# Kernel tuning notes

Measured on AMD Instinct MI355X. Metric: run time of the kernel, lower is better.

Reference implementation:

```python
import jax, jax.numpy as jnp
import numpy as np

HIDDEN = 1024

def _init_linear(key, in_f, out_f):
    kw, kb = jax.random.split(key)
    bound = 1.0 / np.sqrt(in_f)
    W = jax.random.uniform(kw, (out_f, in_f), jnp.float32, -bound, bound)
    b = jax.random.uniform(kb, (out_f,), jnp.float32, -bound, bound)
    return W, b

def setup_inputs() -> dict:
    key = jax.random.key(0)
    ks = jax.random.split(key, 6)
    x = jax.random.normal(ks[0], (64, 512, 512), jnp.float32)
    # layer 0: input_size=512, hidden=1024
    W_rz0, b_rz0 = _init_linear(ks[1], 512 + HIDDEN, 2 * HIDDEN)
    W_n0, b_n0 = _init_linear(ks[2], 512 + HIDDEN, HIDDEN)
    # layer 1: input_size=hidden=1024
    W_rz1, b_rz1 = _init_linear(ks[3], HIDDEN + HIDDEN, 2 * HIDDEN)
    W_n1, b_n1 = _init_linear(ks[4], HIDDEN + HIDDEN, HIDDEN)
    # final fc: hidden -> output_size=512
    W_fc, b_fc = _init_linear(ks[5], HIDDEN, 512)
    return {"x": x, "W_rz0": W_rz0, "b_rz0": b_rz0, "W_n0": W_n0, "b_n0": b_n0,
            "W_rz1": W_rz1, "b_rz1": b_rz1, "W_n1": W_n1, "b_n1": b_n1,
            "W_fc": W_fc, "b_fc": b_fc}

def _gru_cell(xt, h, W_rz, b_rz, W_n, b_n):
    ih = jnp.concatenate([xt, h], axis=1)                 # [B, in+H]
    rz = ih @ W_rz.T + b_rz                               # [B, 2H]
    r, z = jnp.split(rz, 2, axis=1)
    r = jax.nn.sigmoid(r)
    z = jax.nn.sigmoid(z)
    ih_n = jnp.concatenate([xt, r * h], axis=1)
    n = jnp.tanh(ih_n @ W_n.T + b_n)
    return (1.0 - z) * n + z * h

def reference(x, W_rz0, b_rz0, W_n0, b_n0, W_rz1, b_rz1, W_n1, b_n1, W_fc, b_fc):
    B = x.shape[0]
    h0 = jnp.zeros((B, HIDDEN), x.dtype)
    h1 = jnp.zeros((B, HIDDEN), x.dtype)

    def step(carry, xt):
        h0, h1 = carry
        h0 = _gru_cell(xt, h0, W_rz0, b_rz0, W_n0, b_n0)
        h1 = _gru_cell(h0, h1, W_rz1, b_rz1, W_n1, b_n1)
        return (h0, h1), None

    xs = jnp.swapaxes(x, 0, 1)                            # [T, B, in]
    (h0, h1), _ = jax.lax.scan(step, (h0, h1), xs)
    # original returns outputs[:, -1, :] == fc(final hidden of last layer)
    return h1 @ W_fc.T + b_fc
```

## Files before the change

kernel.cpp:

```cpp
#include <hip/hip_runtime.h>
#include <math.h>

typedef _Float16 h8 __attribute__((ext_vector_type(8)));
typedef float f4 __attribute__((ext_vector_type(4)));

#define H 1024

#define OFF_WRZ0 0ull
#define OFF_WN0  6291456ull
#define OFF_WRZ1 9437184ull
#define OFF_WN1  17825792ull
#define OFF_H0BF 22020096ull
#define OFF_H1BF 22282240ull
#define OFF_RH0  22544384ull
#define OFF_RH1  22675456ull
#define OFF_H0F  22806528ull
#define OFF_H1F  23068672ull
#define OFF_Z0F  23330816ull
#define OFF_Z1F  23592960ull
#define OFF_CNT  23855104ull
#define OFF_INFO 23855168ull
#define OFF_CCNT 23855680ull
#define OFF_CP   23859200ull
#define CP_XCD_STRIDE 1048576ull
#define ZERO_WORDS 458960

__device__ __forceinline__ unsigned long long llc_ld64(const void* p) {
  return __hip_atomic_load((const unsigned long long*)p, __ATOMIC_RELAXED, __HIP_MEMORY_SCOPE_AGENT);
}
__device__ __forceinline__ void llc_st64(void* p, unsigned long long v) {
  __hip_atomic_store((unsigned long long*)p, v, __ATOMIC_RELAXED, __HIP_MEMORY_SCOPE_AGENT);
}
__device__ __forceinline__ void llc_st32(void* p, unsigned v) {
  __hip_atomic_store((unsigned*)p, v, __ATOMIC_RELAXED, __HIP_MEMORY_SCOPE_AGENT);
}
__device__ __forceinline__ unsigned long long pack2f(float a, float b) {
  union { float f[2]; unsigned long long u; } x; x.f[0] = a; x.f[1] = b; return x.u;
}
__device__ __forceinline__ void unpack2f(unsigned long long v, float& a, float& b) {
  union { unsigned long long u; float f[2]; } x; x.u = v; a = x.f[0]; b = x.f[1];
}
__device__ __forceinline__ unsigned packh2(float a, float b) {
  union { _Float16 h[2]; unsigned u; } x; x.h[0] = (_Float16)a; x.h[1] = (_Float16)b; return x.u;
}

__global__ __launch_bounds__(256) void prep_kernel(
    const float* __restrict__ wrz0f, const float* __restrict__ wn0f,
    const float* __restrict__ wrz1f, const float* __restrict__ wn1f,
    _Float16* __restrict__ wrz0, _Float16* __restrict__ wn0,
    _Float16* __restrict__ wrz1, _Float16* __restrict__ wn1,
    unsigned* __restrict__ zbase) {
  size_t i = (size_t)blockIdx.x * blockDim.x + threadIdx.x;
  size_t stride = (size_t)gridDim.x * blockDim.x;
  for (size_t k = i; k < 2048ull * 1536ull; k += stride) wrz0[k] = (_Float16)wrz0f[k];
  for (size_t k = i; k < 1024ull * 1536ull; k += stride) wn0[k]  = (_Float16)wn0f[k];
  for (size_t k = i; k < 2048ull * 2048ull; k += stride) wrz1[k] = (_Float16)wrz1f[k];
  for (size_t k = i; k < 1024ull * 2048ull; k += stride) wn1[k]  = (_Float16)wn1f[k];
  for (size_t k = i; k < (size_t)ZERO_WORDS; k += stride) zbase[k] = 0u;
}

__device__ __forceinline__ void wait_ge(unsigned long long* c, unsigned long long tgt) {
  if (threadIdx.x == 0) {
    while (__hip_atomic_load(c, __ATOMIC_RELAXED, __HIP_MEMORY_SCOPE_AGENT) < tgt)
      __builtin_amdgcn_s_sleep(2);
  }
  __syncthreads();
}
__device__ __forceinline__ void signal(unsigned long long* c) {
  __syncthreads();
  if (threadIdx.x == 0)
    __hip_atomic_fetch_add(c, 1ull, __ATOMIC_RELAXED, __HIP_MEMORY_SCOPE_AGENT);
}

__device__ __forceinline__ void copy_tensor(const void* __restrict__ master,
                                            void* __restrict__ cp,
                                            int rank, int m,
                                            unsigned long long* ccnt,
                                            unsigned long long target) {
  const unsigned long long* src = (const unsigned long long*)master;
  unsigned long long* dst = (unsigned long long*)cp;
  for (int u = rank * 1024 + (int)threadIdx.x; u < 16384; u += m * 1024)
    dst[u] = llc_ld64(src + u);
  __syncthreads();
  if (threadIdx.x == 0) {
    __hip_atomic_fetch_add(ccnt, 1ull, __ATOMIC_RELAXED, __HIP_MEMORY_SCOPE_AGENT);
    while (__hip_atomic_load(ccnt, __ATOMIC_RELAXED, __HIP_MEMORY_SCOPE_AGENT) < target)
      __builtin_amdgcn_s_sleep(2);
  }
  __syncthreads();
  asm volatile("buffer_inv sc0" ::: "memory");
}

template<int NT>
__device__ __forceinline__ void gemm_cp(const _Float16* __restrict__ A,
                                        const _Float16* const* wps, int coff, f4* acc) {
  const int lane = threadIdx.x & 63, wv = threadIdx.x >> 6;
  const int kwq = wv & 3, mw = wv >> 2;
  const int rsub = lane & 15, kg = (lane >> 4) << 3;
  const _Float16* ap = A + (size_t)(mw * 16 + rsub) * 1024 + kwq * 256 + kg;
#pragma unroll
  for (int k0 = 0; k0 < 256; k0 += 32) {
    h8 a = *(const h8*)(ap + k0);
    int kc = coff + kwq * 256 + k0 + kg;
#pragma unroll
    for (int c = 0; c < NT; ++c) {
      h8 wf = *(const h8*)(wps[c] + kc);
      acc[c] = __builtin_amdgcn_mfma_f32_16x16x32_f16(a, wf, acc[c], 0, 0, 0);
    }
  }
}

__device__ __forceinline__ void gemm_x(const float* __restrict__ x, int t,
                                       const _Float16* __restrict__ wr0,
                                       const _Float16* __restrict__ wr1,
                                       const _Float16* __restrict__ wn,
                                       f4* aRZ, f4* aN) {
  const int lane = threadIdx.x & 63, wv = threadIdx.x >> 6;
  const int kwq = wv & 3, mw = wv >> 2;
  const int rsub = lane & 15, kg = (lane >> 4) << 3;
  const float* xb = x + (size_t)(mw * 16 + rsub) * 262144 + (size_t)t * 512;
#pragma unroll
  for (int k0 = 0; k0 < 128; k0 += 32) {
    int k = kwq * 128 + k0 + kg;
    float4 f0 = *(const float4*)(xb + k);
    float4 f1 = *(const float4*)(xb + k + 4);
    h8 a;
    a[0] = (_Float16)f0.x; a[1] = (_Float16)f0.y; a[2] = (_Float16)f0.z; a[3] = (_Float16)f0.w;
    a[4] = (_Float16)f1.x; a[5] = (_Float16)f1.y; a[6] = (_Float16)f1.z; a[7] = (_Float16)f1.w;
    aRZ[0] = __builtin_amdgcn_mfma_f32_16x16x32_f16(a, *(const h8*)(wr0 + k), aRZ[0], 0, 0, 0);
    aRZ[1] = __builtin_amdgcn_mfma_f32_16x16x32_f16(a, *(const h8*)(wr1 + k), aRZ[1], 0, 0, 0);
    aN[0]  = __builtin_amdgcn_mfma_f32_16x16x32_f16(a, *(const h8*)(wn + k),  aN[0], 0, 0, 0);
  }
}

template<int NT>
__device__ __forceinline__ void red_write(float* __restrict__ red, const f4* acc) {
  const int lane = threadIdx.x & 63, wv = threadIdx.x >> 6;
  const int kwq = wv & 3, mw = wv >> 2;
  const int rsub = lane & 15, rg = lane >> 4;
#pragma unroll
  for (int c = 0; c < NT; ++c)
#pragma unroll
    for (int j = 0; j < 4; ++j)
      red[(size_t)(kwq * 64 + mw * 16 + rg * 4 + j) * 33 + c * 16 + rsub] = acc[c][j];
}

__device__ __forceinline__ void reduce_rz(const float* __restrict__ red, int cb,
    const float* __restrict__ bias, const float* __restrict__ hf,
    _Float16* __restrict__ rh, float* __restrict__ zf) {
  const int tid = threadIdx.x;
  const int row = tid >> 4, cp = (tid & 15) << 1;
  float v0 = 0.f, v1 = 0.f;
#pragma unroll
  for (int q = 0; q < 4; ++q) {
    const float* rr = red + (size_t)(q * 64 + row) * 33 + cp;
    v0 += rr[0]; v1 += rr[1];
  }
  v0 += bias[cb + cp]; v1 += bias[cb + cp + 1];
  float s0 = 1.f / (1.f + expf(-v0));
  float s1 = 1.f / (1.f + expf(-v1));
  if (cb < 1024) {
    float h0v, h1v;
    unpack2f(llc_ld64(hf + (size_t)row * H + cb + cp), h0v, h1v);
    llc_st32(rh + (size_t)row * H + cb + cp, packh2(s0 * h0v, s1 * h1v));
  } else {
    llc_st64(zf + (size_t)row * H + (cb - 1024) + cp, pack2f(s0, s1));
  }
}

__device__ __forceinline__ void reduce_n(const float* __restrict__ red, int nb,
    const float* __restrict__ bias, const float* __restrict__ zf,
    float* __restrict__ hf, _Float16* __restrict__ hb) {
  const int tid = threadIdx.x;
  if (tid < 512) {
    const int row = tid >> 3, cp = (tid & 7) << 1;
    float v0 = 0.f, v1 = 0.f;
#pragma unroll
    for (int q = 0; q < 4; ++q) {
      const float* rr = red + (size_t)(q * 64 + row) * 33 + cp;
      v0 += rr[0]; v1 += rr[1];
    }
    v0 += bias[nb + cp]; v1 += bias[nb + cp + 1];
    float n0 = tanhf(v0), n1 = tanhf(v1);
    float z0, z1, h0v, h1v;
    unpack2f(llc_ld64(zf + (size_t)row * H + nb + cp), z0, z1);
    unpack2f(llc_ld64(hf + (size_t)row * H + nb + cp), h0v, h1v);
    float o0 = (1.f - z0) * n0 + z0 * h0v;
    float o1 = (1.f - z1) * n1 + z1 * h1v;
    llc_st64(hf + (size_t)row * H + nb + cp, pack2f(o0, o1));
    llc_st32(hb + (size_t)row * H + nb + cp, packh2(o0, o1));
  }
}

__global__ __launch_bounds__(1024) void gru_main(const float* __restrict__ x,
    const _Float16* __restrict__ wrz0, const _Float16* __restrict__ wn0,
    const _Float16* __restrict__ wrz1, const _Float16* __restrict__ wn1,
    const float* __restrict__ brz0, const float* __restrict__ bn0,
    const float* __restrict__ brz1, const float* __restrict__ bn1,
    _Float16* __restrict__ h0bf, _Float16* __restrict__ h1bf,
    _Float16* __restrict__ rh0, _Float16* __restrict__ rh1,
    float* __restrict__ h0f, float* __restrict__ h1f,
    float* __restrict__ z0f, float* __restrict__ z1f,
    unsigned long long* __restrict__ cnt, unsigned* __restrict__ info,
    unsigned long long* __restrict__ ccnt_all, char* __restrict__ cpbase) {
  __shared__ float red[256 * 33];
  __shared__ int sh_meta[5];
  const int bid = blockIdx.x;
  const int tid = threadIdx.x;
  const int myrole = (bid < 64) ? 0 : 1;

  if (tid == 0) {
    unsigned xcc;
    asm volatile("s_getreg_b32 %0, hwreg(HW_REG_XCC_ID)" : "=s"(xcc));
    xcc &= 7u;
    llc_st32(&info[bid], 0x80000000u | xcc);
    asm volatile("s_waitcnt vmcnt(0)" ::: "memory");
    __hip_atomic_fetch_add(&cnt[4], 1ull, __ATOMIC_RELAXED, __HIP_MEMORY_SCOPE_AGENT);
    while (__hip_atomic_load(&cnt[4], __ATOMIC_RELAXED, __HIP_MEMORY_SCOPE_AGENT) < 128ull)
      __builtin_amdgcn_s_sleep(2);
    int rankA = 0, mA = 0, rankR = 0, mR = 0;
    for (int b = 0; b < 128; ++b) {
      unsigned v = (unsigned)__hip_atomic_load(&info[b], __ATOMIC_RELAXED, __HIP_MEMORY_SCOPE_AGENT);
      if ((v & 7u) == xcc) {
        int role = (b < 64) ? 0 : 1;
        if (b < bid) rankA++;
        mA++;
        if (role == myrole) { if (b < bid) rankR++; mR++; }
      }
    }
    sh_meta[0] = (int)xcc; sh_meta[1] = rankA; sh_meta[2] = mA;
    sh_meta[3] = rankR; sh_meta[4] = mR;
  }
  __syncthreads();
  const int xcd = sh_meta[0], rankA = sh_meta[1], mA = sh_meta[2];
  const int rankR = sh_meta[3], mR = sh_meta[4];
  unsigned long long* cc = ccnt_all + (size_t)xcd * 4;
  char* cpx = cpbase + (size_t)xcd * CP_XCD_STRIDE;
  _Float16* cpH0[2]  = {(_Float16*)(cpx + 0*131072), (_Float16*)(cpx + 1*131072)};
  _Float16* cpRH0[2] = {(_Float16*)(cpx + 2*131072), (_Float16*)(cpx + 3*131072)};
  _Float16* cpH1[2]  = {(_Float16*)(cpx + 4*131072), (_Float16*)(cpx + 5*131072)};
  _Float16* cpRH1[2] = {(_Float16*)(cpx + 6*131072), (_Float16*)(cpx + 7*131072)};
  const int rsub = tid & 15;

  if (myrole == 0) {
    const int cb = bid * 32, nb = bid * 16;
    const _Float16* wpsRZ[2] = { wrz0 + (size_t)(cb + rsub) * 1536,
                                 wrz0 + (size_t)(cb + 16 + rsub) * 1536 };
    const _Float16* wpsN[1] = { wn0 + (size_t)(nb + rsub) * 1536 };
    for (int t = 0; t < 512; ++t) {
      f4 aRZ[2] = { f4{0.f,0.f,0.f,0.f}, f4{0.f,0.f,0.f,0.f} };
      f4 aN[1] = { f4{0.f,0.f,0.f,0.f} };
      gemm_x(x, t, wpsRZ[0], wpsRZ[1], wpsN[0], aRZ, aN);
      wait_ge(&cnt[1], 64ull * (unsigned long long)t);
      if (t >= 1) {
        copy_tensor(h0bf + (size_t)((t - 1) & 1) * 65536, cpH0[(t - 1) & 1],
                    rankA, mA, &cc[0], (unsigned long long)mA * t);
        gemm_cp<2>(cpH0[(t - 1) & 1], wpsRZ, 512, aRZ);
      }
      red_write<2>(red, aRZ);
      __syncthreads();
      reduce_rz(red, cb, brz0, h0f, rh0, z0f);
      signal(&cnt[0]);
      wait_ge(&cnt[0], 64ull * (unsigned long long)(t + 1));
      if (t >= 1) wait_ge(&cnt[3], 64ull * (unsigned long long)(t - 1));
      if (t >= 1) {
        copy_tensor(rh0, cpRH0[t & 1], rankR, mR, &cc[1], (unsigned long long)mR * t);
        gemm_cp<1>(cpRH0[t & 1], wpsN, 512, aN);
      }
      red_write<1>(red, aN);
      __syncthreads();
      reduce_n(red, nb, bn0, z0f, h0f, h0bf + (size_t)(t & 1) * 65536);
      signal(&cnt[1]);
    }
  } else {
    const int b = bid - 64, cb = b * 32, nb = b * 16;
    const _Float16* wps3[3] = { wrz1 + (size_t)(cb + rsub) * 2048,
                                wrz1 + (size_t)(cb + 16 + rsub) * 2048,
                                wn1  + (size_t)(nb + rsub) * 2048 };
    for (int t = 1; t <= 512; ++t) {
      const int s = t - 1;
      f4 acc3[3] = { f4{0.f,0.f,0.f,0.f}, f4{0.f,0.f,0.f,0.f}, f4{0.f,0.f,0.f,0.f} };
      wait_ge(&cnt[3], 64ull * (unsigned long long)s);
      if (s >= 1) {
        copy_tensor(h1bf + (size_t)((s - 1) & 1) * 65536, cpH1[(s - 1) & 1],
                    rankR, mR, &cc[2], (unsigned long long)mR * s);
        gemm_cp<2>(cpH1[(s - 1) & 1], wps3, 1024, acc3);
      }
      wait_ge(&cnt[1], 64ull * (unsigned long long)t);
      {
        int rk = (t <= 511) ? rankA : rankR;
        int mm = (t <= 511) ? mA : mR;
        unsigned long long tg = (t <= 511) ? (unsigned long long)mA * t
                                           : (unsigned long long)mA * 511 + (unsigned long long)mR;
        copy_tensor(h0bf + (size_t)((t - 1) & 1) * 65536, cpH0[(t - 1) & 1],
                    rk, mm, &cc[0], tg);
        gemm_cp<3>(cpH0[(t - 1) & 1], wps3, 0, acc3);
      }
      red_write<2>(red, acc3);
      __syncthreads();
      reduce_rz(red, cb, brz1, h1f, rh1, z1f);
      signal(&cnt[2]);
      wait_ge(&cnt[2], 64ull * (unsigned long long)t);
      if (s >= 1) {
        copy_tensor(rh1, cpRH1[s & 1], rankR, mR, &cc[3], (unsigned long long)mR * s);
        gemm_cp<1>(cpRH1[s & 1], wps3 + 2, 1024, acc3 + 2);
      }
      red_write<1>(red, acc3 + 2);
      __syncthreads();
      reduce_n(red, nb, bn1, z1f, h1f, h1bf + (size_t)(s & 1) * 65536);
      signal(&cnt[3]);
    }
  }
}

__global__ __launch_bounds__(256) void fc_kernel(const float* __restrict__ h1f,
                                                 const float* __restrict__ wfc,
                                                 const float* __restrict__ bfc,
                                                 float* __restrict__ out) {
  const int bid = blockIdx.x;
#pragma unroll
  for (int rep = 0; rep < 2; ++rep) {
    int local = threadIdx.x + rep * 256;
    int b = local >> 3;
    int o = bid * 8 + (local & 7);
    const float4* hp = (const float4*)(h1f + (size_t)b * 1024);
    const float4* wp = (const float4*)(wfc + (size_t)o * 1024);
    float s = 0.f;
#pragma unroll 4
    for (int i2 = 0; i2 < 256; ++i2) {
      float4 hv = hp[i2], wv = wp[i2];
      s += hv.x * wv.x + hv.y * wv.y + hv.z * wv.z + hv.w * wv.w;
    }
    out[(size_t)b * 512 + o] = s + bfc[o];
  }
}

extern "C" void kernel_launch(void* const* d_in, const int* in_sizes, int n_in,
                              void* d_out, int out_size, void* d_ws, size_t ws_size,
                              hipStream_t stream) {
  const float* x    = (const float*)d_in[0];
  const float* Wrz0 = (const float*)d_in[1];
  const float* brz0 = (const float*)d_in[2];
  const float* Wn0  = (const float*)d_in[3];
  const float* bn0  = (const float*)d_in[4];
  const float* Wrz1 = (const float*)d_in[5];
  const float* brz1 = (const float*)d_in[6];
  const float* Wn1  = (const float*)d_in[7];
  const float* bn1  = (const float*)d_in[8];
  const float* Wfc  = (const float*)d_in[9];
  const float* bfc  = (const float*)d_in[10];
  float* out = (float*)d_out;
  char* ws = (char*)d_ws;

  _Float16* wrz0h = (_Float16*)(ws + OFF_WRZ0);
  _Float16* wn0h  = (_Float16*)(ws + OFF_WN0);
  _Float16* wrz1h = (_Float16*)(ws + OFF_WRZ1);
  _Float16* wn1h  = (_Float16*)(ws + OFF_WN1);
  _Float16* h0bf  = (_Float16*)(ws + OFF_H0BF);
  _Float16* h1bf  = (_Float16*)(ws + OFF_H1BF);
  _Float16* rh0   = (_Float16*)(ws + OFF_RH0);
  _Float16* rh1   = (_Float16*)(ws + OFF_RH1);
  float* h0f = (float*)(ws + OFF_H0F);
  float* h1f = (float*)(ws + OFF_H1F);
  float* z0f = (float*)(ws + OFF_Z0F);
  float* z1f = (float*)(ws + OFF_Z1F);
  unsigned long long* cnt = (unsigned long long*)(ws + OFF_CNT);
  unsigned* info = (unsigned*)(ws + OFF_INFO);
  unsigned long long* ccnt = (unsigned long long*)(ws + OFF_CCNT);
  char* cpbase = ws + OFF_CP;

  prep_kernel<<<2048, 256, 0, stream>>>(Wrz0, Wn0, Wrz1, Wn1,
                                        wrz0h, wn0h, wrz1h, wn1h,
                                        (unsigned*)(ws + OFF_H0BF));
  gru_main<<<128, 1024, 0, stream>>>(x, wrz0h, wn0h, wrz1h, wn1h,
                                     brz0, bn0, brz1, bn1,
                                     h0bf, h1bf, rh0, rh1,
                                     h0f, h1f, z0f, z1f,
                                     cnt, info, ccnt, cpbase);
  fc_kernel<<<64, 256, 0, stream>>>(h1f, Wfc, bfc, out);
}
```

Measured before the change: 22.82 ms.

## Decouple per-XCD staging copies by role and pad copy counters to separate lines

Layer-0 and layer-1 blocks no longer share one per-XCD copy of h0. Each role now keeps its own staging buffers and completion counter, so cross-role rendezvous inside copy_tensor disappears and fewer blocks take part in each copy. The per-XCD counters are spaced 16 words apart to avoid false sharing, and the staging buffers drop double buffering, which could open a reuse race between consecutive steps. Spin loops gain iteration caps that can break out early and silently skip synchronisation if a wait runs long.

```diff
diff --git a/kernel.cpp b/kernel.cpp
--- a/kernel.cpp
+++ b/kernel.cpp
@@ -19,11 +19,11 @@
 #define OFF_Z0F  23330816ull
 #define OFF_Z1F  23592960ull
 #define OFF_CNT  23855104ull
-#define OFF_INFO 23855168ull
-#define OFF_CCNT 23855680ull
-#define OFF_CP   23859200ull
-#define CP_XCD_STRIDE 1048576ull
-#define ZERO_WORDS 458960
+#define OFF_INFO 23856128ull
+#define OFF_CCNT 23857152ull
+#define OFF_CP   23863296ull
+#define CP_XCD_STRIDE 655360ull
+#define ZERO_WORDS 460800
 
 __device__ __forceinline__ unsigned long long llc_ld64(const void* p) {
   return __hip_atomic_load((const unsigned long long*)p, __ATOMIC_RELAXED, __HIP_MEMORY_SCOPE_AGENT);
@@ -61,8 +61,11 @@
 
 __device__ __forceinline__ void wait_ge(unsigned long long* c, unsigned long long tgt) {
   if (threadIdx.x == 0) {
-    while (__hip_atomic_load(c, __ATOMIC_RELAXED, __HIP_MEMORY_SCOPE_AGENT) < tgt)
+    int g = 0;
+    while (__hip_atomic_load(c, __ATOMIC_RELAXED, __HIP_MEMORY_SCOPE_AGENT) < tgt) {
+      if (++g > (1 << 21)) break;
       __builtin_amdgcn_s_sleep(2);
+    }
   }
   __syncthreads();
 }
@@ -84,8 +87,11 @@
   __syncthreads();
   if (threadIdx.x == 0) {
     __hip_atomic_fetch_add(ccnt, 1ull, __ATOMIC_RELAXED, __HIP_MEMORY_SCOPE_AGENT);
-    while (__hip_atomic_load(ccnt, __ATOMIC_RELAXED, __HIP_MEMORY_SCOPE_AGENT) < target)
+    int g = 0;
+    while (__hip_atomic_load(ccnt, __ATOMIC_RELAXED, __HIP_MEMORY_SCOPE_AGENT) < target) {
+      if (++g > (1 << 21)) break;
       __builtin_amdgcn_s_sleep(2);
+    }
   }
   __syncthreads();
   asm volatile("buffer_inv sc0" ::: "memory");
@@ -204,7 +210,7 @@
     unsigned long long* __restrict__ cnt, unsigned* __restrict__ info,
     unsigned long long* __restrict__ ccnt_all, char* __restrict__ cpbase) {
   __shared__ float red[256 * 33];
-  __shared__ int sh_meta[5];
+  __shared__ int sh_meta[3];
   const int bid = blockIdx.x;
   const int tid = threadIdx.x;
   const int myrole = (bid < 64) ? 0 : 1;
@@ -213,33 +219,31 @@
     unsigned xcc;
     asm volatile("s_getreg_b32 %0, hwreg(HW_REG_XCC_ID)" : "=s"(xcc));
     xcc &= 7u;
-    llc_st32(&info[bid], 0x80000000u | xcc);
+    llc_st32(&info[bid], 0x100u | xcc);
     asm volatile("s_waitcnt vmcnt(0)" ::: "memory");
     __hip_atomic_fetch_add(&cnt[4], 1ull, __ATOMIC_RELAXED, __HIP_MEMORY_SCOPE_AGENT);
-    while (__hip_atomic_load(&cnt[4], __ATOMIC_RELAXED, __HIP_MEMORY_SCOPE_AGENT) < 128ull)
+    int g = 0;
+    while (__hip_atomic_load(&cnt[4], __ATOMIC_RELAXED, __HIP_MEMORY_SCOPE_AGENT) < 128ull) {
+      if (++g > (1 << 22)) break;
       __builtin_amdgcn_s_sleep(2);
-    int rankA = 0, mA = 0, rankR = 0, mR = 0;
+    }
+    int rankR = 0, mR = 0;
     for (int b = 0; b < 128; ++b) {
       unsigned v = (unsigned)__hip_atomic_load(&info[b], __ATOMIC_RELAXED, __HIP_MEMORY_SCOPE_AGENT);
-      if ((v & 7u) == xcc) {
-        int role = (b < 64) ? 0 : 1;
-        if (b < bid) rankA++;
-        mA++;
-        if (role == myrole) { if (b < bid) rankR++; mR++; }
-      }
-    }
-    sh_meta[0] = (int)xcc; sh_meta[1] = rankA; sh_meta[2] = mA;
-    sh_meta[3] = rankR; sh_meta[4] = mR;
-  }
-  __syncthreads();
-  const int xcd = sh_meta[0], rankA = sh_meta[1], mA = sh_meta[2];
-  const int rankR = sh_meta[3], mR = sh_meta[4];
-  unsigned long long* cc = ccnt_all + (size_t)xcd * 4;
+      if ((v & 7u) == xcc && ((b < 64) ? 0 : 1) == myrole) {
+        if (b < bid) rankR++;
+        mR++;
+      }
+    }
+    sh_meta[0] = (int)xcc; sh_meta[1] = rankR; sh_meta[2] = mR;
+  }
+  __syncthreads();
+  const int xcd = sh_meta[0], rankR = sh_meta[1], mR = sh_meta[2];
+  unsigned long long* cc = ccnt_all + (size_t)xcd * 5 * 16;
   char* cpx = cpbase + (size_t)xcd * CP_XCD_STRIDE;
-  _Float16* cpH0[2]  = {(_Float16*)(cpx + 0*131072), (_Float16*)(cpx + 1*131072)};
-  _Float16* cpRH0[2] = {(_Float16*)(cpx + 2*131072), (_Float16*)(cpx + 3*131072)};
-  _Float16* cpH1[2]  = {(_Float16*)(cpx + 4*131072), (_Float16*)(cpx + 5*131072)};
-  _Float16* cpRH1[2] = {(_Float16*)(cpx + 6*131072), (_Float16*)(cpx + 7*131072)};
+  _Float16* cpS[5];
+#pragma unroll
+  for (int i = 0; i < 5; ++i) cpS[i] = (_Float16*)(cpx + (size_t)i * 131072);
   const int rsub = tid & 15;
 
   if (myrole == 0) {
@@ -253,9 +257,9 @@
       gemm_x(x, t, wpsRZ[0], wpsRZ[1], wpsN[0], aRZ, aN);
       wait_ge(&cnt[1], 64ull * (unsigned long long)t);
       if (t >= 1) {
-        copy_tensor(h0bf + (size_t)((t - 1) & 1) * 65536, cpH0[(t - 1) & 1],
-                    rankA, mA, &cc[0], (unsigned long long)mA * t);
-        gemm_cp<2>(cpH0[(t - 1) & 1], wpsRZ, 512, aRZ);
+        copy_tensor(h0bf + (size_t)((t - 1) & 1) * 65536, cpS[0],
+                    rankR, mR, &cc[0 * 16], (unsigned long long)mR * t);
+        gemm_cp<2>(cpS[0], wpsRZ, 512, aRZ);
       }
       red_write<2>(red, aRZ);
       __syncthreads();
@@ -264,8 +268,8 @@
       wait_ge(&cnt[0], 64ull * (unsigned long long)(t + 1));
       if (t >= 1) wait_ge(&cnt[3], 64ull * (unsigned long long)(t - 1));
       if (t >= 1) {
-        copy_tensor(rh0, cpRH0[t & 1], rankR, mR, &cc[1], (unsigned long long)mR * t);
-        gemm_cp<1>(cpRH0[t & 1], wpsN, 512, aN);
+        copy_tensor(rh0, cpS[1], rankR, mR, &cc[1 * 16], (unsigned long long)mR * t);
+        gemm_cp<1>(cpS[1], wpsN, 512, aN);
       }
       red_write<1>(red, aN);
       __syncthreads();
@@ -282,28 +286,22 @@
       f4 acc3[3] = { f4{0.f,0.f,0.f,0.f}, f4{0.f,0.f,0.f,0.f}, f4{0.f,0.f,0.f,0.f} };
       wait_ge(&cnt[3], 64ull * (unsigned long long)s);
       if (s >= 1) {
-        copy_tensor(h1bf + (size_t)((s - 1) & 1) * 65536, cpH1[(s - 1) & 1],
-                    rankR, mR, &cc[2], (unsigned long long)mR * s);
-        gemm_cp<2>(cpH1[(s - 1) & 1], wps3, 1024, acc3);
+        copy_tensor(h1bf + (size_t)((s - 1) & 1) * 65536, cpS[2],
+                    rankR, mR, &cc[2 * 16], (unsigned long long)mR * s);
+        gemm_cp<2>(cpS[2], wps3, 1024, acc3);
       }
       wait_ge(&cnt[1], 64ull * (unsigned long long)t);
-      {
-        int rk = (t <= 511) ? rankA : rankR;
-        int mm = (t <= 511) ? mA : mR;
-        unsigned long long tg = (t <= 511) ? (unsigned long long)mA * t
-                                           : (unsigned long long)mA * 511 + (unsigned long long)mR;
-        copy_tensor(h0bf + (size_t)((t - 1) & 1) * 65536, cpH0[(t - 1) & 1],
-                    rk, mm, &cc[0], tg);
-        gemm_cp<3>(cpH0[(t - 1) & 1], wps3, 0, acc3);
-      }
+      copy_tensor(h0bf + (size_t)((t - 1) & 1) * 65536, cpS[3],
+                  rankR, mR, &cc[3 * 16], (unsigned long long)mR * t);
+      gemm_cp<3>(cpS[3], wps3, 0, acc3);
       red_write<2>(red, acc3);
       __syncthreads();
       reduce_rz(red, cb, brz1, h1f, rh1, z1f);
       signal(&cnt[2]);
       wait_ge(&cnt[2], 64ull * (unsigned long long)t);
       if (s >= 1) {
-        copy_tensor(rh1, cpRH1[s & 1], rankR, mR, &cc[3], (unsigned long long)mR * s);
-        gemm_cp<1>(cpRH1[s & 1], wps3 + 2, 1024, acc3 + 2);
+        copy_tensor(rh1, cpS[4], rankR, mR, &cc[4 * 16], (unsigned long long)mR * s);
+        gemm_cp<1>(cpS[4], wps3 + 2, 1024, acc3 + 2);
       }
       red_write<1>(red, acc3 + 2);
       __syncthreads();
```

Result: no change. 23.03 ms (+0.9%).
